# Kernel tuning notes

Measured on AMD Instinct MI355X. Metric: run time of the kernel, lower is better.

The kernel has to match this reference:

```python
import jax, jax.numpy as jnp
import numpy as np

N, E, G = 10000, 100000, 16
NS, NV = 128, 64            # scalar (0e) / vector (1o) channel counts
DIM = NS + 3 * NV           # 320 flattened feature dim
NSP = 4                     # num_species; edge one-hot has NSP**2 entries
FC_IN = 128                 # edge length embedding size
GATES = NV                  # one gate scalar per gated vector channel
EPS = 1e-5


def _split(x):
    # flattened irreps layout: [NS scalars | NV vectors * 3 components]
    return x[:, :NS], x[:, NS:].reshape(x.shape[0], NV, 3)


def _merge(s, v):
    return jnp.concatenate([s, v.reshape(v.shape[0], -1)], axis=-1)


def setup_inputs() -> dict:
    key = jax.random.key(0)
    ks = jax.random.split(key, 32)
    def nrm(i, shape):
        return jax.random.normal(ks[i], shape, jnp.float32)
    return {
        'node_fea': nrm(0, (N, DIM)),
        'edge_one_hot': jax.random.uniform(ks[1], (E, NSP * NSP), jnp.float32),
        'edge_sh': nrm(2, (E, 4)),
        'edge_fea': nrm(3, (E, DIM)),
        'edge_length_embedded': jax.random.uniform(ks[4], (E, FC_IN), jnp.float32),
        'edge_index': jax.random.randint(ks[5], (2, E), 0, N),
        'batch': jnp.sort(jax.random.randint(ks[6], (N,), 0, G)),
        # self-connection FCTP: edge irreps x species-pair scalars -> out irreps
        'Wsc_s': nrm(7, (NS, NSP * NSP, NS)),
        'Wsc_v': nrm(8, (NV, NSP * NSP, NV)),
        # lin_pre (per-l equivariant linear, bias on scalars only)
        'Wpre0': nrm(9, (NS, NS)), 'bpre0': jnp.zeros((NS,), jnp.float32),
        'Wpre1': nrm(10, (NV, NV)),
        # separate-weight tensor product paths (fea_in x spherical harmonics)
        'Wss': nrm(11, (3 * NS, NS + GATES)),   # 0e x 0e -> 0e
        'Wvs': nrm(12, (3 * NV, NS + GATES)),   # 1o . 1o -> 0e
        'Wsv': nrm(13, (3 * NS, NV)),           # 0e x 1o -> 1o
        'Wvv': nrm(14, (3 * NV, NV)),           # 1o x 0e -> 1o
        # radial MLP (fc): edge_length_embedded -> per-channel conv weights
        'Wf1': nrm(15, (FC_IN, 64)) / np.sqrt(FC_IN), 'bf1': jnp.zeros((64,), jnp.float32),
        'Wf2': nrm(16, (64, 64)) / 8.0, 'bf2': jnp.zeros((64,), jnp.float32),
        'Wf3': nrm(17, (64, NS + NV)) / 8.0, 'bf3': jnp.zeros((NS + NV,), jnp.float32),
        # lin_post
        'Wpost0': nrm(18, (NS, NS)), 'bpost0': jnp.zeros((NS,), jnp.float32),
        'Wpost1': nrm(19, (NV, NV)),
        # e3LayerNorm affine params
        'gamma_s': jnp.ones((NS,), jnp.float32), 'beta_s': jnp.zeros((NS,), jnp.float32),
        'gamma_v': jnp.ones((NV,), jnp.float32),
    }


def reference(node_fea, edge_one_hot, edge_sh, edge_fea, edge_length_embedded,
              edge_index, batch, Wsc_s, Wsc_v, Wpre0, bpre0, Wpre1,
              Wss, Wvs, Wsv, Wvv, Wf1, bf1, Wf2, bf2, Wf3, bf3,
              Wpost0, bpost0, Wpost1, gamma_s, beta_s, gamma_v):
    i, j = edge_index[0], edge_index[1]
    batch_edge = batch[i]
    es, ev = _split(edge_fea)

    # --- self connection: FullyConnectedTensorProduct(edge_fea, one_hot) ---
    sc_s = jnp.einsum('ev,es,vsu->eu', es, edge_one_hot, Wsc_s) / np.sqrt(NS * NSP * NSP)
    sc_v = jnp.einsum('evm,es,vsu->eum', ev, edge_one_hot, Wsc_v) / np.sqrt(NV * NSP * NSP)

    # --- lin_pre on edge features ---
    s = es @ Wpre0 / np.sqrt(NS) + bpre0
    v = jnp.einsum('evm,vu->eum', ev, Wpre1) / np.sqrt(NV)

    # --- gather node features and concat along channel axis ---
    nsf, nvf = _split(node_fea)
    s_in = jnp.concatenate([nsf[i], nsf[j], s], axis=-1)   # [E, 3*NS]
    v_in = jnp.concatenate([nvf[i], nvf[j], v], axis=1)    # [E, 3*NV, 3]

    sh0, sh1 = edge_sh[:, :1], edge_sh[:, 1:4]
    # --- separate-weight tensor product (CG: 1o x 1o -> 0e via dot/sqrt(3)) ---
    out_s = (jnp.einsum('ev,vu->eu', s_in * sh0, Wss) / np.sqrt(3 * NS)
             + jnp.einsum('evm,em,vu->eu', v_in, sh1, Wvs) / np.sqrt(3 * 3 * NV)) / np.sqrt(2.0)
    out_v = (jnp.einsum('ev,em,vu->eum', s_in, sh1, Wsv) / np.sqrt(3 * NS)
             + jnp.einsum('evm,e,vu->eum', v_in, sh0[:, 0], Wvv) / np.sqrt(3 * NV)) / np.sqrt(2.0)

    # --- gate nonlinearity: silu on scalars, sigmoid gates on vectors ---
    z_s = jax.nn.silu(out_s[:, :NS])
    z_v = out_v * jax.nn.sigmoid(out_s[:, NS:])[:, :, None]

    # --- radial MLP -> e3ElementWise per-channel scaling ---
    h = jax.nn.silu(edge_length_embedded @ Wf1 + bf1)
    h = jax.nn.silu(h @ Wf2 + bf2)
    w = h @ Wf3 + bf3                                      # [E, NS+NV]
    z_s = z_s * w[:, :NS]
    z_v = z_v * w[:, NS:, None]

    # --- lin_post ---
    z_s = z_s @ Wpost0 / np.sqrt(NS) + bpost0
    z_v = jnp.einsum('evm,vu->eum', z_v, Wpost1) / np.sqrt(NV)

    # --- add self connection ---
    z_s = z_s + sc_s
    z_v = z_v + sc_v

    # --- e3LayerNorm with per-graph statistics over edges ---
    cnt = jax.ops.segment_sum(jnp.ones((E,), z_s.dtype), batch_edge, num_segments=G)
    cnt = jnp.maximum(cnt, 1.0)
    mean_s = jax.ops.segment_sum(z_s.sum(-1), batch_edge, num_segments=G) / (cnt * NS)
    z_s = z_s - mean_s[batch_edge][:, None]
    var_s = jax.ops.segment_sum((z_s ** 2).sum(-1), batch_edge, num_segments=G) / (cnt * NS)
    z_s = z_s * jax.lax.rsqrt(var_s + EPS)[batch_edge][:, None] * gamma_s + beta_s
    var_v = jax.ops.segment_sum((z_v ** 2).sum((-1, -2)), batch_edge, num_segments=G) / (cnt * NV * 3)
    z_v = z_v * jax.lax.rsqrt(var_v + EPS)[batch_edge][:, None, None] * gamma_v[None, :, None]

    # --- skip connection (same irreps in/out -> plain add) ---
    return edge_fea + _merge(z_s, z_v)
```

## Files before the change

### kernel.cpp

```cpp
#include <hip/hip_runtime.h>
#include <math.h>

typedef unsigned int u32;
typedef unsigned short u16;
typedef __attribute__((ext_vector_type(8))) short bf16x8;
typedef __attribute__((ext_vector_type(4))) float f32x4;

#define E_TOT 100000
constexpr int NS = 128, DIM = 320;

constexpr float SC_S_SCALE = 0.022097086912079608f;
constexpr float SC_V_SCALE = 0.03125f;
constexpr float INV_SQRT128 = 0.08838834764831845f;
constexpr float INV_8 = 0.125f;
constexpr float INV_S384 = 0.05103103630798288f;
constexpr float INV_24 = 0.041666666666666664f;
constexpr float INV_S192 = 0.07216878364870323f;
constexpr float RSQRT2 = 0.7071067811865476f;

#define MFMA __builtin_amdgcn_mfma_f32_16x16x32_bf16
#define F4Z (f32x4){0.f, 0.f, 0.f, 0.f}

__device__ __forceinline__ float sigmoidf_(float x) { return 1.0f / (1.0f + __expf(-x)); }
__device__ __forceinline__ float siluf_(float x) { return x * sigmoidf_(x); }
__device__ __forceinline__ float bf2f(u16 h) {
  u32 u = ((u32)h) << 16;
  return __builtin_bit_cast(float, u);
}
__device__ __forceinline__ u16 f2bf(float f) {
  u32 u = __builtin_bit_cast(u32, f);
  return (u16)((u + 0x7fffu + ((u >> 16) & 1u)) >> 16);
}
__device__ __forceinline__ void gl_lds16(const void* g, void* l) {
  __builtin_amdgcn_global_load_lds((const __attribute__((address_space(1))) u32*)g,
                                   (__attribute__((address_space(3))) u32*)l, 16, 0, 0);
}
__device__ __forceinline__ bf16x8 pack8(float4 r0, float4 r1, float s) {
  bf16x8 a;
  a[0] = (short)f2bf(r0.x * s); a[1] = (short)f2bf(r0.y * s);
  a[2] = (short)f2bf(r0.z * s); a[3] = (short)f2bf(r0.w * s);
  a[4] = (short)f2bf(r1.x * s); a[5] = (short)f2bf(r1.y * s);
  a[6] = (short)f2bf(r1.z * s); a[7] = (short)f2bf(r1.w * s);
  return a;
}
__device__ __forceinline__ void stb(char* base, int row, int rowB, int colByte, u16 v) {
  *(u16*)(base + row * rowB + (colByte ^ ((row & 7) << 4))) = v;
}
__device__ __forceinline__ u16 ldbs(const char* base, int row, int rowB, int colByte) {
  return *(const u16*)(base + row * rowB + (colByte ^ ((row & 7) << 4)));
}
__device__ __forceinline__ bf16x8 ldb8(const char* base, int row, int rowB, int colByte) {
  return *(const bf16x8*)(base + row * rowB + (colByte ^ ((row & 7) << 4)));
}
__device__ __forceinline__ void stb16(char* base, int row, int rowB, int colByte, bf16x8 v) {
  *(bf16x8*)(base + row * rowB + (colByte ^ ((row & 7) << 4))) = v;
}
__device__ __forceinline__ bf16x8 scale8_sh1(bf16x8 v, int m0, float t0, float t1, float t2) {
  float x0 = (m0 == 0) ? t0 : ((m0 == 1) ? t1 : t2);
  float x1 = (m0 == 0) ? t1 : ((m0 == 1) ? t2 : t0);
  float x2 = (m0 == 0) ? t2 : ((m0 == 1) ? t0 : t1);
  bf16x8 r;
  r[0] = (short)f2bf(bf2f((u16)v[0]) * x0); r[1] = (short)f2bf(bf2f((u16)v[1]) * x1);
  r[2] = (short)f2bf(bf2f((u16)v[2]) * x2); r[3] = (short)f2bf(bf2f((u16)v[3]) * x0);
  r[4] = (short)f2bf(bf2f((u16)v[4]) * x1); r[5] = (short)f2bf(bf2f((u16)v[5]) * x2);
  r[6] = (short)f2bf(bf2f((u16)v[6]) * x0); r[7] = (short)f2bf(bf2f((u16)v[7]) * x1);
  return r;
}

#define OW_W2S   0
#define OW_BTV   262144
#define OW_PRE0  327680
#define OW_PRE1X 344064
#define OW_SS    380928
#define OW_VSX   454656
#define OW_SV    565248
#define OW_VVX   589824
#define OW_F1    700416
#define OW_F2    708608
#define OW_F3    712704
#define OW_P0    724992
#define OW_P1X   741376
#define OW_END   778240

__device__ __forceinline__ void frag_uc(int oo, int K, int& up, int& c) {
  int per = (K >> 5) << 9;
  int nt = oo / per, r = oo % per;
  int kc = r >> 9, r2 = r & 511;
  int ln = r2 >> 3, j = r2 & 7;
  up = nt * 16 + (ln & 15);
  c = kc * 32 + (ln >> 4) * 8 + j;
}

__global__ __launch_bounds__(256) void k_prep(
    const float* __restrict__ Wsc_s, const float* __restrict__ Wsc_v,
    const float* __restrict__ Wpre0, const float* __restrict__ Wpre1,
    const float* __restrict__ Wss, const float* __restrict__ Wvs,
    const float* __restrict__ Wsv, const float* __restrict__ Wvv,
    const float* __restrict__ Wf1, const float* __restrict__ Wf2,
    const float* __restrict__ Wf3, const float* __restrict__ Wpost0,
    const float* __restrict__ Wpost1, u16* __restrict__ dst) {
  int o = blockIdx.x * 256 + threadIdx.x;
  if (o >= OW_END) return;
  float v;
  int up, c;
  if (o < OW_BTV) {
    int u = o >> 11, k = o & 2047, s = k >> 7, vv = k & 127;
    v = Wsc_s[((size_t)(vv * 16 + s)) * 128 + u] * SC_S_SCALE;
  } else if (o < OW_PRE0) {
    int oo = o - OW_BTV; int u = oo >> 10, k = oo & 1023, s = k >> 6, vv = k & 63;
    v = Wsc_v[((size_t)(vv * 16 + s)) * 64 + u] * SC_V_SCALE;
  } else if (o < OW_PRE1X) {
    frag_uc(o - OW_PRE0, 128, up, c);
    v = Wpre0[c * 128 + up] * INV_SQRT128;
  } else if (o < OW_SS) {
    frag_uc(o - OW_PRE1X, 192, up, c);
    int u = up / 3, m = up % 3, vv = c / 3, mp = c % 3;
    v = (m == mp) ? Wpre1[vv * 64 + u] * INV_8 : 0.f;
  } else if (o < OW_VSX) {
    frag_uc(o - OW_SS, 384, up, c);
    v = Wss[c * 192 + up] * (INV_S384 * RSQRT2);
  } else if (o < OW_SV) {
    frag_uc(o - OW_VSX, 576, up, c);
    int p = c / 192, r = c % 192, K = p * 64 + r / 3;
    v = Wvs[K * 192 + up] * (INV_24 * RSQRT2);
  } else if (o < OW_VVX) {
    frag_uc(o - OW_SV, 384, up, c);
    v = Wsv[c * 64 + up] * (INV_S384 * RSQRT2);
  } else if (o < OW_F1) {
    frag_uc(o - OW_VVX, 576, up, c);
    int u = up / 3, m = up % 3, p = c / 192, r = c % 192, vv = r / 3, mp = r % 3;
    v = (m == mp) ? Wvv[(p * 64 + vv) * 64 + u] * (INV_S192 * RSQRT2) : 0.f;
  } else if (o < OW_F2) {
    frag_uc(o - OW_F1, 128, up, c);
    v = Wf1[c * 64 + up];
  } else if (o < OW_F3) {
    frag_uc(o - OW_F2, 64, up, c);
    v = Wf2[c * 64 + up];
  } else if (o < OW_P0) {
    frag_uc(o - OW_F3, 64, up, c);
    v = Wf3[c * 192 + up];
  } else if (o < OW_P1X) {
    frag_uc(o - OW_P0, 128, up, c);
    v = Wpost0[c * 128 + up] * INV_SQRT128;
  } else {
    frag_uc(o - OW_P1X, 192, up, c);
    int u = up / 3, m = up % 3, vv = c / 3, mp = c % 3;
    v = (m == mp) ? Wpost1[vv * 64 + u] * INV_8 : 0.f;
  }
  dst[o] = f2bf(v);
}

#define MEs 64
__global__ __launch_bounds__(256, 2) void k_sc(
    const float* __restrict__ edge_fea, const float* __restrict__ ohp,
    const u16* __restrict__ W2s, const u16* __restrict__ Btv,
    float* __restrict__ out) {
  __shared__ char esB[16384];
  __shared__ char evT[24576];
  __shared__ float ohL[64][16];
  __shared__ char Bbuf[32768];
  const int t = threadIdx.x, lane = t & 63, ww = t >> 6;
  const int l15 = lane & 15, q8 = lane >> 4, q4 = q8 << 2, cbl = q8 << 4;
  const int e0 = blockIdx.x * MEs;
  const int nE = min(MEs, E_TOT - e0);

  for (int o = t; o < 2560; o += 256) {
    int c = o % 40, e = o / 40;
    float4 r0 = make_float4(0.f, 0.f, 0.f, 0.f), r1 = r0;
    if (e < nE) {
      const float* src = edge_fea + (size_t)(e0 + e) * 320 + c * 8;
      r0 = *(const float4*)src; r1 = *(const float4*)(src + 4);
    }
    if (c < 16) stb16(esB, e, 256, c * 16, pack8(r0, r1, 1.f));
    else {
      int base = (c - 16) * 8;
      float vals[8] = {r0.x, r0.y, r0.z, r0.w, r1.x, r1.y, r1.z, r1.w};
      #pragma unroll
      for (int z = 0; z < 8; ++z) {
        int cc = base + z;
        stb(evT, 3 * e + cc % 3, 128, (cc / 3) * 2, f2bf(vals[z]));
      }
    }
  }
  for (int o = t; o < 1024; o += 256) {
    int e = o >> 4, s = o & 15;
    ohL[e][s] = (e < nE) ? ohp[(size_t)(e0 + e) * 16 + s] : 0.f;
  }
  __syncthreads();

  {
    bf16x8 afh[4][4];
    #pragma unroll
    for (int rt = 0; rt < 4; ++rt)
      #pragma unroll
      for (int ks = 0; ks < 4; ++ks)
        afh[rt][ks] = ldb8(esB, rt * 16 + l15, 256, ks * 64 + cbl);
    f32x4 acc[8];
    #pragma unroll
    for (int i = 0; i < 8; ++i) acc[i] = F4Z;
    for (int s = 0; s < 16; ++s) {
      const char* sb = (const char*)W2s + s * 256;
      #pragma unroll
      for (int it = 0; it < 8; ++it) {
        int n = it * 256 + t;
        int u = n >> 4, gp = n & 15, g = gp ^ (u & 7);
        gl_lds16(sb + (size_t)u * 4096 + g * 16, Bbuf + n * 16);
      }
      __syncthreads();
      f32x4 tmp[8];
      #pragma unroll
      for (int i = 0; i < 8; ++i) tmp[i] = F4Z;
      #pragma unroll
      for (int ks = 0; ks < 4; ++ks) {
        bf16x8 b0 = ldb8(Bbuf, ww * 32 + l15, 256, ks * 64 + cbl);
        bf16x8 b1 = ldb8(Bbuf, ww * 32 + 16 + l15, 256, ks * 64 + cbl);
        #pragma unroll
        for (int rt = 0; rt < 4; ++rt) {
          tmp[rt * 2 + 0] = MFMA(afh[rt][ks], b0, tmp[rt * 2 + 0], 0, 0, 0);
          tmp[rt * 2 + 1] = MFMA(afh[rt][ks], b1, tmp[rt * 2 + 1], 0, 0, 0);
        }
      }
      #pragma unroll
      for (int rt = 0; rt < 4; ++rt)
        #pragma unroll
        for (int j = 0; j < 4; ++j) {
          float oh = ohL[rt * 16 + q4 + j][s];
          acc[rt * 2 + 0][j] += oh * tmp[rt * 2 + 0][j];
          acc[rt * 2 + 1][j] += oh * tmp[rt * 2 + 1][j];
        }
      __syncthreads();
    }
    #pragma unroll
    for (int rt = 0; rt < 4; ++rt)
      #pragma unroll
      for (int ct = 0; ct < 2; ++ct) {
        int u = ww * 32 + ct * 16 + l15;
        #pragma unroll
        for (int j = 0; j < 4; ++j) {
          int e = rt * 16 + q4 + j;
          if (e < nE) out[(size_t)(e0 + e) * DIM + u] = acc[rt * 2 + ct][j];
        }
      }
  }

  {
    f32x4 acc[12];
    #pragma unroll
    for (int i = 0; i < 12; ++i) acc[i] = F4Z;
    for (int s = 0; s < 16; ++s) {
      #pragma unroll
      for (int it = 0; it < 2; ++it) {
        int n = it * 256 + t;
        int u = n >> 3, gp = n & 7, g = gp ^ (u & 7);
        gl_lds16((const char*)Btv + (size_t)u * 2048 + s * 128 + g * 16, Bbuf + n * 16);
      }
      __syncthreads();
      f32x4 tmp[12];
      #pragma unroll
      for (int i = 0; i < 12; ++i) tmp[i] = F4Z;
      #pragma unroll
      for (int ks = 0; ks < 2; ++ks) {
        bf16x8 b = ldb8(Bbuf, ww * 16 + l15, 128, ks * 64 + cbl);
        #pragma unroll
        for (int rt = 0; rt < 12; ++rt) {
          bf16x8 a = ldb8(evT, rt * 16 + l15, 128, ks * 64 + cbl);
          tmp[rt] = MFMA(a, b, tmp[rt], 0, 0, 0);
        }
      }
      #pragma unroll
      for (int rt = 0; rt < 12; ++rt)
        #pragma unroll
        for (int j = 0; j < 4; ++j) {
          int r = rt * 16 + q4 + j;
          acc[rt][j] += ohL[r / 3][s] * tmp[rt][j];
        }
      __syncthreads();
    }
    int u = ww * 16 + l15;
    #pragma unroll
    for (int rt = 0; rt < 12; ++rt)
      #pragma unroll
      for (int j = 0; j < 4; ++j) {
        int r = rt * 16 + q4 + j, e = r / 3, m = r - e * 3;
        if (e < nE) out[(size_t)(e0 + e) * DIM + 128 + u * 3 + m] = acc[rt][j];
      }
  }
}

#define A_SZ 78592
__global__ __launch_bounds__(512, 4) void k_chain(
    const float* __restrict__ node_fea, const float* __restrict__ edge_sh,
    const float* __restrict__ edge_fea, const float* __restrict__ elen,
    const int* __restrict__ eidx, const u16* __restrict__ wbf,
    const float* __restrict__ bpre0, const float* __restrict__ bf1,
    const float* __restrict__ bf2, const float* __restrict__ bf3,
    const float* __restrict__ bpost0, float* __restrict__ out) {
  __shared__ char AR[A_SZ];
  float* shF = (float*)(AR + 77824);
  int* ijL = (int*)(AR + 78336);
  const int t = threadIdx.x, lane = t & 63, wv = t >> 6;
  const int l15 = lane & 15, q8 = lane >> 4, q4 = q8 << 2, cbl = q8 << 4;
  const int e0 = blockIdx.x * 32;

#define SA(b) (AR + (b) * 8192)
#define VA(b) (AR + 24576 + (b) * 12288)
  char* wB = AR;
  char* zsB = AR + 12288;
  char* gateB = AR + 20480;
  char* zvB = AR + 24576;
  char* t1B = AR + 61440;
  char* hB = AR + 65536;
  char* elB = AR + 69632;

  if (t < 64) { int p = t >> 5, e = t & 31; ijL[p * 32 + e] = eidx[p * E_TOT + e0 + e]; }
  if (t >= 64 && t < 192) { int o = t - 64; shF[o] = edge_sh[(size_t)e0 * 4 + o]; }
  __syncthreads();

  for (int o = t; o < 1280; o += 512) {
    int c = o % 40, e = o / 40;
    const float* src = edge_fea + (size_t)(e0 + e) * 320 + c * 8;
    float4 r0 = *(const float4*)src, r1 = *(const float4*)(src + 4);
    bf16x8 v = pack8(r0, r1, 1.f);
    if (c < 16) stb16(SA(2), e, 256, c * 16, v);
    else        stb16(VA(2), e, 384, (c - 16) * 16, v);
  }
  for (int o = t; o < 2560; o += 512) {
    int c = o % 40, tmp = o / 40, e = tmp & 31, p = tmp >> 5;
    const float* src = node_fea + (size_t)ijL[p * 32 + e] * 320 + c * 8;
    float4 r0 = *(const float4*)src, r1 = *(const float4*)(src + 4);
    bf16x8 v = pack8(r0, r1, 1.f);
    if (c < 16) stb16(SA(p), e, 256, c * 16, v);
    else        stb16(VA(p), e, 384, (c - 16) * 16, v);
  }
  for (int o = t; o < 512; o += 512) {
    int c = o & 15, e = o >> 4;
    const float* src = elen + (size_t)(e0 + e) * 128 + c * 8;
    float4 r0 = *(const float4*)src, r1 = *(const float4*)(src + 4);
    stb16(elB, e, 256, c * 16, pack8(r0, r1, 1.f));
  }
  __syncthreads();

  f32x4 acc[8];
  #pragma unroll
  for (int a = 0; a < 8; ++a) acc[a] = F4Z;
  if (wv < 4) {
    for (int kc = 0; kc < 6; ++kc) {
      bf16x8 a0 = ldb8(VA(2), l15, 384, kc * 64 + cbl);
      bf16x8 a1 = ldb8(VA(2), 16 + l15, 384, kc * 64 + cbl);
      #pragma unroll
      for (int i = 0; i < 3; ++i) {
        int nt = wv * 3 + i;
        bf16x8 b = *(const bf16x8*)(wbf + OW_PRE1X + (((size_t)nt * 6 + kc) << 9) + lane * 8);
        acc[i] = MFMA(a0, b, acc[i], 0, 0, 0);
        acc[3 + i] = MFMA(a1, b, acc[3 + i], 0, 0, 0);
      }
    }
  } else if (wv < 6) {
    for (int kc = 0; kc < 4; ++kc) {
      bf16x8 a0 = ldb8(SA(2), l15, 256, kc * 64 + cbl);
      bf16x8 a1 = ldb8(SA(2), 16 + l15, 256, kc * 64 + cbl);
      #pragma unroll
      for (int i = 0; i < 4; ++i) {
        int nt = (wv - 4) * 4 + i;
        bf16x8 b = *(const bf16x8*)(wbf + OW_PRE0 + (((size_t)nt * 4 + kc) << 9) + lane * 8);
        acc[i] = MFMA(a0, b, acc[i], 0, 0, 0);
        acc[4 + i] = MFMA(a1, b, acc[4 + i], 0, 0, 0);
      }
    }
  } else {
    for (int kc = 0; kc < 4; ++kc) {
      bf16x8 a0 = ldb8(elB, l15, 256, kc * 64 + cbl);
      bf16x8 a1 = ldb8(elB, 16 + l15, 256, kc * 64 + cbl);
      #pragma unroll
      for (int i = 0; i < 2; ++i) {
        int nt = (wv - 6) * 2 + i;
        bf16x8 b = *(const bf16x8*)(wbf + OW_F1 + (((size_t)nt * 4 + kc) << 9) + lane * 8);
        acc[i] = MFMA(a0, b, acc[i], 0, 0, 0);
        acc[2 + i] = MFMA(a1, b, acc[2 + i], 0, 0, 0);
      }
    }
  }
  __syncthreads();
  if (wv < 4) {
    #pragma unroll
    for (int mt = 0; mt < 2; ++mt)
      #pragma unroll
      for (int i = 0; i < 3; ++i) {
        int up = (wv * 3 + i) * 16 + l15;
        #pragma unroll
        for (int j = 0; j < 4; ++j)
          stb(VA(2), mt * 16 + q4 + j, 384, up * 2, f2bf(acc[mt * 3 + i][j]));
      }
  } else if (wv < 6) {
    #pragma unroll
    for (int i = 0; i < 4; ++i) {
      int u = ((wv - 4) * 4 + i) * 16 + l15;
      float bias = bpre0[u];
      #pragma unroll
      for (int mt = 0; mt < 2; ++mt)
        #pragma unroll
        for (int j = 0; j < 4; ++j)
          stb(SA(2), mt * 16 + q4 + j, 256, u * 2, f2bf(acc[mt * 4 + i][j] + bias));
    }
  } else {
    #pragma unroll
    for (int i = 0; i < 2; ++i) {
      int u = ((wv - 6) * 2 + i) * 16 + l15;
      float bias = bf1[u];
      #pragma unroll
      for (int mt = 0; mt < 2; ++mt)
        #pragma unroll
        for (int j = 0; j < 4; ++j)
          stb(hB, mt * 16 + q4 + j, 128, u * 2, f2bf(siluf_(acc[mt * 2 + i][j] + bias)));
    }
  }
  __syncthreads();

  f32x4 os[4] = {F4Z, F4Z, F4Z, F4Z};
  f32x4 h2a = F4Z;
  {
    const int hmt = wv >> 2, hnt = wv & 3;
    #pragma unroll
    for (int kc = 0; kc < 2; ++kc) {
      bf16x8 a = ldb8(hB, hmt * 16 + l15, 128, kc * 64 + cbl);
      bf16x8 b = *(const bf16x8*)(wbf + OW_F2 + (((size_t)hnt * 2 + kc) << 9) + lane * 8);
      h2a = MFMA(a, b, h2a, 0, 0, 0);
    }
  }
  if (wv < 6) {
    for (int kc = 0; kc < 12; ++kc) {
      int buf = kc >> 2, cB = (kc & 3) * 64 + cbl;
      bf16x8 a0 = ldb8(SA(buf), l15, 256, cB);
      bf16x8 a1 = ldb8(SA(buf), 16 + l15, 256, cB);
      #pragma unroll
      for (int i = 0; i < 2; ++i) {
        int nt = wv * 2 + i;
        bf16x8 b = *(const bf16x8*)(wbf + OW_SS + (((size_t)nt * 12 + kc) << 9) + lane * 8);
        os[i] = MFMA(a0, b, os[i], 0, 0, 0);
        os[2 + i] = MFMA(a1, b, os[2 + i], 0, 0, 0);
      }
    }
    #pragma unroll
    for (int mt = 0; mt < 2; ++mt)
      #pragma unroll
      for (int i = 0; i < 2; ++i)
        #pragma unroll
        for (int j = 0; j < 4; ++j)
          os[mt * 2 + i][j] *= shF[(mt * 16 + q4 + j) * 4 + 0];
    float sa0 = shF[l15 * 4 + 1], sa1 = shF[l15 * 4 + 2], sa2 = shF[l15 * 4 + 3];
    float sb0 = shF[(16 + l15) * 4 + 1], sb1 = shF[(16 + l15) * 4 + 2], sb2 = shF[(16 + l15) * 4 + 3];
    for (int p = 0; p < 3; ++p)
      for (int kc6 = 0; kc6 < 6; ++kc6) {
        int cB = kc6 * 64 + cbl;
        int m0 = (2 * (kc6 + q8)) % 3;
        bf16x8 a0 = scale8_sh1(ldb8(VA(p), l15, 384, cB), m0, sa0, sa1, sa2);
        bf16x8 a1 = scale8_sh1(ldb8(VA(p), 16 + l15, 384, cB), m0, sb0, sb1, sb2);
        int kcg = p * 6 + kc6;
        #pragma unroll
        for (int i = 0; i < 2; ++i) {
          int nt = wv * 2 + i;
          bf16x8 b = *(const bf16x8*)(wbf + OW_VSX + (((size_t)nt * 18 + kcg) << 9) + lane * 8);
          os[i] = MFMA(a0, b, os[i], 0, 0, 0);
          os[2 + i] = MFMA(a1, b, os[2 + i], 0, 0, 0);
        }
      }
  } else {
    for (int kc = 0; kc < 12; ++kc) {
      int buf = kc >> 2, cB = (kc & 3) * 64 + cbl;
      bf16x8 a0 = ldb8(SA(buf), l15, 256, cB);
      bf16x8 a1 = ldb8(SA(buf), 16 + l15, 256, cB);
      #pragma unroll
      for (int i = 0; i < 2; ++i) {
        int nt = (wv - 6) * 2 + i;
        bf16x8 b = *(const bf16x8*)(wbf + OW_SV + (((size_t)nt * 12 + kc) << 9) + lane * 8);
        os[i] = MFMA(a0, b, os[i], 0, 0, 0);
        os[2 + i] = MFMA(a1, b, os[2 + i], 0, 0, 0);
      }
    }
  }
  __syncthreads();
  {
    const int hmt = wv >> 2;
    int u = (wv & 3) * 16 + l15;
    float bias = bf2[u];
    #pragma unroll
    for (int j = 0; j < 4; ++j)
      stb(hB, hmt * 16 + q4 + j, 128, u * 2, f2bf(siluf_(h2a[j] + bias)));
  }
  if (wv >= 6) {
    #pragma unroll
    for (int mt = 0; mt < 2; ++mt)
      #pragma unroll
      for (int i = 0; i < 2; ++i) {
        int u = ((wv - 6) * 2 + i) * 16 + l15;
        #pragma unroll
        for (int j = 0; j < 4; ++j)
          stb(t1B, mt * 16 + q4 + j, 128, u * 2, f2bf(os[mt * 2 + i][j]));
      }
  }
  __syncthreads();

  {
    f32x4 wa[3] = {F4Z, F4Z, F4Z};
    const int mtw = wv >> 2;
    #pragma unroll
    for (int kc = 0; kc < 2; ++kc) {
      bf16x8 a = ldb8(hB, mtw * 16 + l15, 128, kc * 64 + cbl);
      #pragma unroll
      for (int i = 0; i < 3; ++i) {
        int nt = (wv & 3) * 3 + i;
        bf16x8 b = *(const bf16x8*)(wbf + OW_F3 + (((size_t)nt * 2 + kc) << 9) + lane * 8);
        wa[i] = MFMA(a, b, wa[i], 0, 0, 0);
      }
    }
    #pragma unroll
    for (int i = 0; i < 3; ++i) {
      int up = ((wv & 3) * 3 + i) * 16 + l15;
      float bias = bf3[up];
      #pragma unroll
      for (int j = 0; j < 4; ++j)
        stb(wB, mtw * 16 + q4 + j, 384, up * 2, f2bf(wa[i][j] + bias));
    }
  }
  __syncthreads();

  if (wv < 6) {
    #pragma unroll
    for (int mt = 0; mt < 2; ++mt)
      #pragma unroll
      for (int i = 0; i < 2; ++i) {
        int up = (wv * 2 + i) * 16 + l15;
        #pragma unroll
        for (int j = 0; j < 4; ++j) {
          int e = mt * 16 + q4 + j;
          float w_ = bf2f(ldbs(wB, e, 384, up * 2));
          float o_ = os[mt * 2 + i][j];
          if (up < 128) stb(zsB, e, 256, up * 2, f2bf(siluf_(o_) * w_));
          else stb(gateB, e, 128, (up - 128) * 2, f2bf(sigmoidf_(o_) * w_));
        }
      }
  }
  f32x4 ov[3] = {F4Z, F4Z, F4Z};
  {
    const int mtv = wv >> 2;
    for (int p = 0; p < 3; ++p)
      for (int kc6 = 0; kc6 < 6; ++kc6) {
        int cB = kc6 * 64 + cbl;
        bf16x8 a = ldb8(VA(p), mtv * 16 + l15, 384, cB);
        int kcg = p * 6 + kc6;
        #pragma unroll
        for (int i = 0; i < 3; ++i) {
          int nt = (wv & 3) * 3 + i;
          bf16x8 b = *(const bf16x8*)(wbf + OW_VVX + (((size_t)nt * 18 + kcg) << 9) + lane * 8);
          ov[i] = MFMA(a, b, ov[i], 0, 0, 0);
        }
      }
  }
  __syncthreads();
  {
    const int mtv = wv >> 2;
    #pragma unroll
    for (int i = 0; i < 3; ++i) {
      int up = ((wv & 3) * 3 + i) * 16 + l15;
      int u = (up * 683) >> 11, m = up - 3 * u;
      #pragma unroll
      for (int j = 0; j < 4; ++j) {
        int e = mtv * 16 + q4 + j;
        float t1v = bf2f(ldbs(t1B, e, 128, u * 2));
        float g = bf2f(ldbs(gateB, e, 128, u * 2));
        float val = ov[i][j] * shF[e * 4 + 0] + t1v * shF[e * 4 + 1 + m];
        stb(zvB, e, 384, up * 2, f2bf(val * g));
      }
    }
  }
  __syncthreads();

  {
    f32x4 p0[2] = {F4Z, F4Z};
    #pragma unroll
    for (int kc = 0; kc < 4; ++kc) {
      int cB = kc * 64 + cbl;
      bf16x8 a0 = ldb8(zsB, l15, 256, cB);
      bf16x8 a1 = ldb8(zsB, 16 + l15, 256, cB);
      bf16x8 b = *(const bf16x8*)(wbf + OW_P0 + (((size_t)wv * 4 + kc) << 9) + lane * 8);
      p0[0] = MFMA(a0, b, p0[0], 0, 0, 0);
      p0[1] = MFMA(a1, b, p0[1], 0, 0, 0);
    }
    int u = wv * 16 + l15;
    float bias = bpost0[u];
    #pragma unroll
    for (int mt = 0; mt < 2; ++mt)
      #pragma unroll
      for (int j = 0; j < 4; ++j) {
        size_t o = (size_t)(e0 + mt * 16 + q4 + j) * DIM + u;
        out[o] = out[o] + p0[mt][j] + bias;
      }
  }
  {
    f32x4 p1[3] = {F4Z, F4Z, F4Z};
    const int mtv = wv >> 2;
    #pragma unroll
    for (int kc = 0; kc < 6; ++kc) {
      int cB = kc * 64 + cbl;
      bf16x8 a = ldb8(zvB, mtv * 16 + l15, 384, cB);
      #pragma unroll
      for (int i = 0; i < 3; ++i) {
        int nt = (wv & 3) * 3 + i;
        bf16x8 b = *(const bf16x8*)(wbf + OW_P1X + (((size_t)nt * 6 + kc) << 9) + lane * 8);
        p1[i] = MFMA(a, b, p1[i], 0, 0, 0);
      }
    }
    #pragma unroll
    for (int i = 0; i < 3; ++i) {
      int up = ((wv & 3) * 3 + i) * 16 + l15;
      #pragma unroll
      for (int j = 0; j < 4; ++j) {
        size_t o = (size_t)(e0 + mtv * 16 + q4 + j) * DIM + 128 + up;
        out[o] = out[o] + p1[i][j];
      }
    }
  }
#undef SA
#undef VA
}

__global__ __launch_bounds__(256) void k_stats(
    const float* __restrict__ out, const int* __restrict__ eidx,
    const int* __restrict__ batch, float* __restrict__ stats) {
  __shared__ float gacc[16][4];
  const int t = threadIdx.x;
  if (t < 64) ((float*)gacc)[t] = 0.0f;
  __syncthreads();
  const int el = t >> 4, l = t & 15;
  for (int ebase = blockIdx.x * 16; ebase < E_TOT; ebase += gridDim.x * 16) {
    int e = ebase + el;
    const float4* z4 = (const float4*)(out + (size_t)e * DIM);
    float s1 = 0, s2 = 0, s2v = 0;
    float4 a = z4[l], b = z4[16 + l];
    s1 = a.x + a.y + a.z + a.w + b.x + b.y + b.z + b.w;
    s2 = a.x * a.x + a.y * a.y + a.z * a.z + a.w * a.w +
         b.x * b.x + b.y * b.y + b.z * b.z + b.w * b.w;
    #pragma unroll
    for (int p = 0; p < 3; ++p) {
      float4 c = z4[32 + p * 16 + l];
      s2v += c.x * c.x + c.y * c.y + c.z * c.z + c.w * c.w;
    }
    #pragma unroll
    for (int msk = 8; msk; msk >>= 1) {
      s1 += __shfl_xor(s1, msk);
      s2 += __shfl_xor(s2, msk);
      s2v += __shfl_xor(s2v, msk);
    }
    if (l == 0) {
      int g = batch[eidx[e]];
      atomicAdd(&gacc[g][0], 1.0f);
      atomicAdd(&gacc[g][1], s1);
      atomicAdd(&gacc[g][2], s2);
      atomicAdd(&gacc[g][3], s2v);
    }
  }
  __syncthreads();
  if (t < 64) {
    float v = gacc[t >> 2][t & 3];
    if (v != 0.0f) atomicAdd(&stats[(t >> 2) * 16 + (t & 3)], v);
  }
}

__global__ __launch_bounds__(256) void k_norm(
    const float* __restrict__ edge_fea, const int* __restrict__ eidx,
    const int* __restrict__ batch, const float* __restrict__ stats,
    const float* __restrict__ gamma_s, const float* __restrict__ beta_s,
    const float* __restrict__ gamma_v, float* __restrict__ out) {
  __shared__ float meanL[16], invsL[16], invvL[16];
  __shared__ int gL[16];
  const int t = threadIdx.x;
  const int e0 = blockIdx.x * 16;
  if (t < 16) {
    float cnt = fmaxf(stats[t * 16 + 0], 1.0f);
    float m = stats[t * 16 + 1] / (cnt * 128.0f);
    float var = stats[t * 16 + 2] / (cnt * 128.0f) - m * m;
    meanL[t] = m;
    invsL[t] = rsqrtf(var + 1e-5f);
    invvL[t] = rsqrtf(stats[t * 16 + 3] / (cnt * 192.0f) + 1e-5f);
  }
  if (t >= 32 && t < 48) gL[t - 32] = batch[eidx[e0 + t - 32]];
  __syncthreads();
  for (int o = t; o < 16 * 80; o += 256) {
    int e = o / 80, q = o % 80;
    size_t idx = (size_t)(e0 + e) * 80 + q;
    float4 z = ((const float4*)out)[idx];
    float4 ef = ((const float4*)edge_fea)[idx];
    int g = gL[e];
    float4 r;
    if (q < 32) {
      int c = q * 4;
      r.x = (z.x - meanL[g]) * invsL[g] * gamma_s[c + 0] + beta_s[c + 0] + ef.x;
      r.y = (z.y - meanL[g]) * invsL[g] * gamma_s[c + 1] + beta_s[c + 1] + ef.y;
      r.z = (z.z - meanL[g]) * invsL[g] * gamma_s[c + 2] + beta_s[c + 2] + ef.z;
      r.w = (z.w - meanL[g]) * invsL[g] * gamma_s[c + 3] + beta_s[c + 3] + ef.w;
    } else {
      int cc = q * 4 - 128;
      r.x = z.x * invvL[g] * gamma_v[(cc + 0) / 3] + ef.x;
      r.y = z.y * invvL[g] * gamma_v[(cc + 1) / 3] + ef.y;
      r.z = z.z * invvL[g] * gamma_v[(cc + 2) / 3] + ef.z;
      r.w = z.w * invvL[g] * gamma_v[(cc + 3) / 3] + ef.w;
    }
    ((float4*)out)[idx] = r;
  }
}

extern "C" void kernel_launch(void* const* d_in, const int* in_sizes, int n_in,
                              void* d_out, int out_size, void* d_ws, size_t ws_size,
                              hipStream_t stream) {
  const float* node_fea = (const float*)d_in[0];
  const float* edge_oh  = (const float*)d_in[1];
  const float* edge_sh  = (const float*)d_in[2];
  const float* edge_fea = (const float*)d_in[3];
  const float* elen     = (const float*)d_in[4];
  const int*   eidx     = (const int*)d_in[5];
  const int*   batch    = (const int*)d_in[6];
  const float* Wsc_s    = (const float*)d_in[7];
  const float* Wsc_v    = (const float*)d_in[8];
  const float* Wpre0    = (const float*)d_in[9];
  const float* bpre0    = (const float*)d_in[10];
  const float* Wpre1    = (const float*)d_in[11];
  const float* Wss      = (const float*)d_in[12];
  const float* Wvs      = (const float*)d_in[13];
  const float* Wsv      = (const float*)d_in[14];
  const float* Wvv      = (const float*)d_in[15];
  const float* Wf1      = (const float*)d_in[16];
  const float* bf1      = (const float*)d_in[17];
  const float* Wf2      = (const float*)d_in[18];
  const float* bf2      = (const float*)d_in[19];
  const float* Wf3      = (const float*)d_in[20];
  const float* bf3      = (const float*)d_in[21];
  const float* Wpost0   = (const float*)d_in[22];
  const float* bpost0   = (const float*)d_in[23];
  const float* Wpost1   = (const float*)d_in[24];
  const float* gamma_s  = (const float*)d_in[25];
  const float* beta_s   = (const float*)d_in[26];
  const float* gamma_v  = (const float*)d_in[27];
  float* out = (float*)d_out;

  char* ws = (char*)d_ws;
  float* stats = (float*)ws;
  u16* wbf = (u16*)(ws + 1024);

  hipMemsetAsync(stats, 0, 16 * 16 * sizeof(float), stream);
  k_prep<<<(OW_END + 255) / 256, 256, 0, stream>>>(
      Wsc_s, Wsc_v, Wpre0, Wpre1, Wss, Wvs, Wsv, Wvv,
      Wf1, Wf2, Wf3, Wpost0, Wpost1, wbf);
  const int nblk64 = (E_TOT + MEs - 1) / MEs;
  k_sc<<<nblk64, 256, 0, stream>>>(edge_fea, edge_oh, wbf + OW_W2S, wbf + OW_BTV, out);
  k_chain<<<E_TOT / 32, 512, 0, stream>>>(node_fea, edge_sh, edge_fea, elen, eidx,
                                          wbf, bpre0, bf1, bf2, bf3, bpost0, out);
  k_stats<<<512, 256, 0, stream>>>(out, eidx, batch, stats);
  k_norm<<<E_TOT / 16, 256, 0, stream>>>(edge_fea, eidx, batch, stats,
                                         gamma_s, beta_s, gamma_v, out);
}
```

Before: 659.2 us.

## Fuse LayerNorm statistics into chain kernel and precontract vector-sh dot product

The separate statistics kernel, which re-read the whole output, is removed. Per-edge sums, squared sums and vector squared sums are now reduced inside the chain kernel's epilogue and written into 64 bucketed per-graph partials, which the norm kernel sums. Separately, the 1o·1o→0e path first contracts vectors with the spherical harmonics into a 192-wide buffer, so the matmul runs over K=192 instead of 576 and the expanded weight block shrinks. This adds shared-memory atomics, an extra pass and a synchronisation in the chain kernel. The norm kernel also now loops over 64 partial buckets per graph.

```diff
diff --git a/kernel.cpp b/kernel.cpp
--- a/kernel.cpp
+++ b/kernel.cpp
@@ -55,32 +55,21 @@
 __device__ __forceinline__ void stb16(char* base, int row, int rowB, int colByte, bf16x8 v) {
   *(bf16x8*)(base + row * rowB + (colByte ^ ((row & 7) << 4))) = v;
 }
-__device__ __forceinline__ bf16x8 scale8_sh1(bf16x8 v, int m0, float t0, float t1, float t2) {
-  float x0 = (m0 == 0) ? t0 : ((m0 == 1) ? t1 : t2);
-  float x1 = (m0 == 0) ? t1 : ((m0 == 1) ? t2 : t0);
-  float x2 = (m0 == 0) ? t2 : ((m0 == 1) ? t0 : t1);
-  bf16x8 r;
-  r[0] = (short)f2bf(bf2f((u16)v[0]) * x0); r[1] = (short)f2bf(bf2f((u16)v[1]) * x1);
-  r[2] = (short)f2bf(bf2f((u16)v[2]) * x2); r[3] = (short)f2bf(bf2f((u16)v[3]) * x0);
-  r[4] = (short)f2bf(bf2f((u16)v[4]) * x1); r[5] = (short)f2bf(bf2f((u16)v[5]) * x2);
-  r[6] = (short)f2bf(bf2f((u16)v[6]) * x0); r[7] = (short)f2bf(bf2f((u16)v[7]) * x1);
-  return r;
-}
 
 #define OW_W2S   0
 #define OW_BTV   262144
 #define OW_PRE0  327680
 #define OW_PRE1X 344064
 #define OW_SS    380928
-#define OW_VSX   454656
-#define OW_SV    565248
-#define OW_VVX   589824
-#define OW_F1    700416
-#define OW_F2    708608
-#define OW_F3    712704
-#define OW_P0    724992
-#define OW_P1X   741376
-#define OW_END   778240
+#define OW_VS    454656
+#define OW_SV    491520
+#define OW_VVX   516096
+#define OW_F1    626688
+#define OW_F2    634880
+#define OW_F3    638976
+#define OW_P0    651264
+#define OW_P1X   667648
+#define OW_END   704512
 
 __device__ __forceinline__ void frag_uc(int oo, int K, int& up, int& c) {
   int per = (K >> 5) << 9;
@@ -116,13 +105,12 @@
     frag_uc(o - OW_PRE1X, 192, up, c);
     int u = up / 3, m = up % 3, vv = c / 3, mp = c % 3;
     v = (m == mp) ? Wpre1[vv * 64 + u] * INV_8 : 0.f;
-  } else if (o < OW_VSX) {
+  } else if (o < OW_VS) {
     frag_uc(o - OW_SS, 384, up, c);
     v = Wss[c * 192 + up] * (INV_S384 * RSQRT2);
   } else if (o < OW_SV) {
-    frag_uc(o - OW_VSX, 576, up, c);
-    int p = c / 192, r = c % 192, K = p * 64 + r / 3;
-    v = Wvs[K * 192 + up] * (INV_24 * RSQRT2);
+    frag_uc(o - OW_VS, 192, up, c);
+    v = Wvs[c * 192 + up] * (INV_24 * RSQRT2);
   } else if (o < OW_VVX) {
     frag_uc(o - OW_SV, 384, up, c);
     v = Wsv[c * 64 + up] * (INV_S384 * RSQRT2);
@@ -287,17 +275,22 @@
   }
 }
 
-#define A_SZ 78592
+#define A_SZ 78976
 __global__ __launch_bounds__(512, 4) void k_chain(
     const float* __restrict__ node_fea, const float* __restrict__ edge_sh,
     const float* __restrict__ edge_fea, const float* __restrict__ elen,
-    const int* __restrict__ eidx, const u16* __restrict__ wbf,
+    const int* __restrict__ eidx, const int* __restrict__ batch,
+    const u16* __restrict__ wbf,
     const float* __restrict__ bpre0, const float* __restrict__ bf1,
     const float* __restrict__ bf2, const float* __restrict__ bf3,
-    const float* __restrict__ bpost0, float* __restrict__ out) {
+    const float* __restrict__ bpost0, float* __restrict__ out,
+    float* __restrict__ statsB) {
   __shared__ char AR[A_SZ];
   float* shF = (float*)(AR + 77824);
   int* ijL = (int*)(AR + 78336);
+  float* sS  = (float*)(AR + 78592);
+  float* sS2 = (float*)(AR + 78720);
+  float* sV  = (float*)(AR + 78848);
   const int t = threadIdx.x, lane = t & 63, wv = t >> 6;
   const int l15 = lane & 15, q8 = lane >> 4, q4 = q8 << 2, cbl = q8 << 4;
   const int e0 = blockIdx.x * 32;
@@ -314,6 +307,7 @@
 
   if (t < 64) { int p = t >> 5, e = t & 31; ijL[p * 32 + e] = eidx[p * E_TOT + e0 + e]; }
   if (t >= 64 && t < 192) { int o = t - 64; shF[o] = edge_sh[(size_t)e0 * 4 + o]; }
+  if (t >= 192 && t < 288) ((float*)(AR + 78592))[t - 192] = 0.f;
   __syncthreads();
 
   for (int o = t; o < 1280; o += 512) {
@@ -416,6 +410,19 @@
   }
   __syncthreads();
 
+  for (int o = t; o < 32 * 192; o += 512) {
+    int e = o / 192, K = o % 192;
+    int src = K >> 6, kk = K & 63;
+    const char* vb = VA(src);
+    float x0 = bf2f(ldbs(vb, e, 384, (3 * kk + 0) * 2));
+    float x1 = bf2f(ldbs(vb, e, 384, (3 * kk + 1) * 2));
+    float x2 = bf2f(ldbs(vb, e, 384, (3 * kk + 2) * 2));
+    float sv = x0 * shF[e * 4 + 1] + x1 * shF[e * 4 + 2] + x2 * shF[e * 4 + 3];
+    if (K < 128) stb(elB, e, 256, K * 2, f2bf(sv));
+    else stb(t1B, e, 128, (K - 128) * 2, f2bf(sv));
+  }
+  __syncthreads();
+
   f32x4 os[4] = {F4Z, F4Z, F4Z, F4Z};
   f32x4 h2a = F4Z;
   {
@@ -447,23 +454,20 @@
         #pragma unroll
         for (int j = 0; j < 4; ++j)
           os[mt * 2 + i][j] *= shF[(mt * 16 + q4 + j) * 4 + 0];
-    float sa0 = shF[l15 * 4 + 1], sa1 = shF[l15 * 4 + 2], sa2 = shF[l15 * 4 + 3];
-    float sb0 = shF[(16 + l15) * 4 + 1], sb1 = shF[(16 + l15) * 4 + 2], sb2 = shF[(16 + l15) * 4 + 3];
-    for (int p = 0; p < 3; ++p)
-      for (int kc6 = 0; kc6 < 6; ++kc6) {
-        int cB = kc6 * 64 + cbl;
-        int m0 = (2 * (kc6 + q8)) % 3;
-        bf16x8 a0 = scale8_sh1(ldb8(VA(p), l15, 384, cB), m0, sa0, sa1, sa2);
-        bf16x8 a1 = scale8_sh1(ldb8(VA(p), 16 + l15, 384, cB), m0, sb0, sb1, sb2);
-        int kcg = p * 6 + kc6;
-        #pragma unroll
-        for (int i = 0; i < 2; ++i) {
-          int nt = wv * 2 + i;
-          bf16x8 b = *(const bf16x8*)(wbf + OW_VSX + (((size_t)nt * 18 + kcg) << 9) + lane * 8);
-          os[i] = MFMA(a0, b, os[i], 0, 0, 0);
-          os[2 + i] = MFMA(a1, b, os[2 + i], 0, 0, 0);
-        }
-      }
+    for (int kc = 0; kc < 6; ++kc) {
+      const char* sb_ = (kc < 4) ? elB : t1B;
+      int rB = (kc < 4) ? 256 : 128;
+      int cB = ((kc < 4) ? kc : (kc - 4)) * 64 + cbl;
+      bf16x8 a0 = ldb8(sb_, l15, rB, cB);
+      bf16x8 a1 = ldb8(sb_, 16 + l15, rB, cB);
+      #pragma unroll
+      for (int i = 0; i < 2; ++i) {
+        int nt = wv * 2 + i;
+        bf16x8 b = *(const bf16x8*)(wbf + OW_VS + (((size_t)nt * 6 + kc) << 9) + lane * 8);
+        os[i] = MFMA(a0, b, os[i], 0, 0, 0);
+        os[2 + i] = MFMA(a1, b, os[2 + i], 0, 0, 0);
+      }
+    }
   } else {
     for (int kc = 0; kc < 12; ++kc) {
       int buf = kc >> 2, cB = (kc & 3) * 64 + cbl;
@@ -588,13 +592,34 @@
     }
     int u = wv * 16 + l15;
     float bias = bpost0[u];
+    float s1p[8], s2p[8];
     #pragma unroll
     for (int mt = 0; mt < 2; ++mt)
       #pragma unroll
       for (int j = 0; j < 4; ++j) {
         size_t o = (size_t)(e0 + mt * 16 + q4 + j) * DIM + u;
-        out[o] = out[o] + p0[mt][j] + bias;
-      }
+        float z = out[o] + p0[mt][j] + bias;
+        out[o] = z;
+        s1p[mt * 4 + j] = z;
+        s2p[mt * 4 + j] = z * z;
+      }
+    #pragma unroll
+    for (int msk = 1; msk < 16; msk <<= 1)
+      #pragma unroll
+      for (int k = 0; k < 8; ++k) {
+        s1p[k] += __shfl_xor(s1p[k], msk);
+        s2p[k] += __shfl_xor(s2p[k], msk);
+      }
+    if (l15 == 0) {
+      #pragma unroll
+      for (int mt = 0; mt < 2; ++mt)
+        #pragma unroll
+        for (int j = 0; j < 4; ++j) {
+          int e = mt * 16 + q4 + j;
+          atomicAdd(&sS[e], s1p[mt * 4 + j]);
+          atomicAdd(&sS2[e], s2p[mt * 4 + j]);
+        }
+    }
   }
   {
     f32x4 p1[3] = {F4Z, F4Z, F4Z};
@@ -610,60 +635,39 @@
         p1[i] = MFMA(a, b, p1[i], 0, 0, 0);
       }
     }
+    float svp[4] = {0.f, 0.f, 0.f, 0.f};
     #pragma unroll
     for (int i = 0; i < 3; ++i) {
       int up = ((wv & 3) * 3 + i) * 16 + l15;
       #pragma unroll
       for (int j = 0; j < 4; ++j) {
         size_t o = (size_t)(e0 + mtv * 16 + q4 + j) * DIM + 128 + up;
-        out[o] = out[o] + p1[i][j];
-      }
-    }
+        float z = out[o] + p1[i][j];
+        out[o] = z;
+        svp[j] += z * z;
+      }
+    }
+    #pragma unroll
+    for (int msk = 1; msk < 16; msk <<= 1)
+      #pragma unroll
+      for (int j = 0; j < 4; ++j) svp[j] += __shfl_xor(svp[j], msk);
+    if (l15 == 0) {
+      #pragma unroll
+      for (int j = 0; j < 4; ++j)
+        atomicAdd(&sV[mtv * 16 + q4 + j], svp[j]);
+    }
+  }
+  __syncthreads();
+  if (t < 32) {
+    int g = batch[ijL[t]];
+    float* sb = statsB + ((size_t)(blockIdx.x & 63)) * 64 + g * 4;
+    atomicAdd(sb + 0, 1.0f);
+    atomicAdd(sb + 1, sS[t]);
+    atomicAdd(sb + 2, sS2[t]);
+    atomicAdd(sb + 3, sV[t]);
   }
 #undef SA
 #undef VA
-}
-
-__global__ __launch_bounds__(256) void k_stats(
-    const float* __restrict__ out, const int* __restrict__ eidx,
-    const int* __restrict__ batch, float* __restrict__ stats) {
-  __shared__ float gacc[16][4];
-  const int t = threadIdx.x;
-  if (t < 64) ((float*)gacc)[t] = 0.0f;
-  __syncthreads();
-  const int el = t >> 4, l = t & 15;
-  for (int ebase = blockIdx.x * 16; ebase < E_TOT; ebase += gridDim.x * 16) {
-    int e = ebase + el;
-    const float4* z4 = (const float4*)(out + (size_t)e * DIM);
-    float s1 = 0, s2 = 0, s2v = 0;
-    float4 a = z4[l], b = z4[16 + l];
-    s1 = a.x + a.y + a.z + a.w + b.x + b.y + b.z + b.w;
-    s2 = a.x * a.x + a.y * a.y + a.z * a.z + a.w * a.w +
-         b.x * b.x + b.y * b.y + b.z * b.z + b.w * b.w;
-    #pragma unroll
-    for (int p = 0; p < 3; ++p) {
-      float4 c = z4[32 + p * 16 + l];
-      s2v += c.x * c.x + c.y * c.y + c.z * c.z + c.w * c.w;
-    }
-    #pragma unroll
-    for (int msk = 8; msk; msk >>= 1) {
-      s1 += __shfl_xor(s1, msk);
-      s2 += __shfl_xor(s2, msk);
-      s2v += __shfl_xor(s2v, msk);
-    }
-    if (l == 0) {
-      int g = batch[eidx[e]];
-      atomicAdd(&gacc[g][0], 1.0f);
-      atomicAdd(&gacc[g][1], s1);
-      atomicAdd(&gacc[g][2], s2);
-      atomicAdd(&gacc[g][3], s2v);
-    }
-  }
-  __syncthreads();
-  if (t < 64) {
-    float v = gacc[t >> 2][t & 3];
-    if (v != 0.0f) atomicAdd(&stats[(t >> 2) * 16 + (t & 3)], v);
-  }
 }
 
 __global__ __launch_bounds__(256) void k_norm(
@@ -676,12 +680,17 @@
   const int t = threadIdx.x;
   const int e0 = blockIdx.x * 16;
   if (t < 16) {
-    float cnt = fmaxf(stats[t * 16 + 0], 1.0f);
-    float m = stats[t * 16 + 1] / (cnt * 128.0f);
-    float var = stats[t * 16 + 2] / (cnt * 128.0f) - m * m;
+    float c = 0.f, a = 0.f, b = 0.f, d = 0.f;
+    for (int q = 0; q < 64; ++q) {
+      const float* p = stats + (size_t)q * 64 + t * 4;
+      c += p[0]; a += p[1]; b += p[2]; d += p[3];
+    }
+    float cnt = fmaxf(c, 1.0f);
+    float m = a / (cnt * 128.0f);
+    float var = b / (cnt * 128.0f) - m * m;
     meanL[t] = m;
     invsL[t] = rsqrtf(var + 1e-5f);
-    invvL[t] = rsqrtf(stats[t * 16 + 3] / (cnt * 192.0f) + 1e-5f);
+    invvL[t] = rsqrtf(d / (cnt * 192.0f) + 1e-5f);
   }
   if (t >= 32 && t < 48) gL[t - 32] = batch[eidx[e0 + t - 32]];
   __syncthreads();
@@ -743,18 +752,17 @@
   float* out = (float*)d_out;
 
   char* ws = (char*)d_ws;
-  float* stats = (float*)ws;
-  u16* wbf = (u16*)(ws + 1024);
-
-  hipMemsetAsync(stats, 0, 16 * 16 * sizeof(float), stream);
+  float* statsB = (float*)ws;
+  u16* wbf = (u16*)(ws + 16384);
+
+  hipMemsetAsync(statsB, 0, 64 * 64 * sizeof(float), stream);
   k_prep<<<(OW_END + 255) / 256, 256, 0, stream>>>(
       Wsc_s, Wsc_v, Wpre0, Wpre1, Wss, Wvs, Wsv, Wvv,
       Wf1, Wf2, Wf3, Wpost0, Wpost1, wbf);
   const int nblk64 = (E_TOT + MEs - 1) / MEs;
   k_sc<<<nblk64, 256, 0, stream>>>(edge_fea, edge_oh, wbf + OW_W2S, wbf + OW_BTV, out);
-  k_chain<<<E_TOT / 32, 512, 0, stream>>>(node_fea, edge_sh, edge_fea, elen, eidx,
-                                          wbf, bpre0, bf1, bf2, bf3, bpost0, out);
-  k_stats<<<512, 256, 0, stream>>>(out, eidx, batch, stats);
-  k_norm<<<E_TOT / 16, 256, 0, stream>>>(edge_fea, eidx, batch, stats,
+  k_chain<<<E_TOT / 32, 512, 0, stream>>>(node_fea, edge_sh, edge_fea, elen, eidx, batch,
+                                          wbf, bpre0, bf1, bf2, bf3, bpost0, out, statsB);
+  k_norm<<<E_TOT / 16, 256, 0, stream>>>(edge_fea, eidx, batch, statsB,
                                          gamma_s, beta_s, gamma_v, out);
 }
```

Result: no change. 652.7 us, median of 3 (-1.0%).
